# Performance work log

Hardware: AMD Instinct MI355X
Metric: run time of the kernel (lower is better)

The kernel has to match this reference:

```python
import jax, jax.numpy as jnp
import numpy as np

N_NODES = 100000
N_EDGES = 1600000
IN_CH = 512
MID_CH = 64   # hard-coded mid_layer_channel in the module
OUT_CH = 40


def setup_inputs() -> dict:
    key = jax.random.key(0)
    k0, k1, k2, k3 = jax.random.split(key, 4)
    node_feature = jax.random.normal(k0, (N_NODES, IN_CH), dtype=jnp.float32)
    # edge index [2, E]: row 0 = src, row 1 = dst
    adj_list = jax.random.randint(k1, (2, N_EDGES), 0, N_NODES, dtype=jnp.int32)
    # GCNConv parameters (Glorot-ish scale)
    W1 = jax.random.normal(k2, (IN_CH, MID_CH), dtype=jnp.float32) * (1.0 / np.sqrt(IN_CH))
    b1 = jnp.zeros((MID_CH,), dtype=jnp.float32)
    W2 = jax.random.normal(k3, (MID_CH, OUT_CH), dtype=jnp.float32) * (1.0 / np.sqrt(MID_CH))
    b2 = jnp.zeros((OUT_CH,), dtype=jnp.float32)
    return {"node_feature": node_feature, "adj_list": adj_list,
            "W1": W1, "b1": b1, "W2": W2, "b2": b2}


def _gcn_conv(x, W, b, src, dst, deg_inv_sqrt, n_nodes):
    # Standard GCNConv: D^{-1/2} (A + I) D^{-1/2} (x W) + b
    h = x @ W                                             # [N, F_out]
    norm = deg_inv_sqrt[src] * deg_inv_sqrt[dst]          # [E]
    agg = jax.ops.segment_sum(h[src] * norm[:, None], dst, num_segments=n_nodes)
    agg = agg + h * (deg_inv_sqrt * deg_inv_sqrt)[:, None]  # self-loop term
    return agg + b


def reference(node_feature, adj_list, W1, b1, W2, b2):
    n = node_feature.shape[0]
    src, dst = adj_list[0], adj_list[1]
    # degree with self-loops (in-degree at dst + 1)
    deg = jax.ops.segment_sum(jnp.ones_like(dst, dtype=node_feature.dtype), dst,
                              num_segments=n) + 1.0
    deg_inv_sqrt = jax.lax.rsqrt(deg)
    h = jax.nn.elu(_gcn_conv(node_feature, W1, b1, src, dst, deg_inv_sqrt, n))
    out = _gcn_conv(h, W2, b2, src, dst, deg_inv_sqrt, n)
    return jax.nn.log_softmax(out, axis=1)
```

## Files before the change

kernel.cpp:

```cpp
#include <hip/hip_runtime.h>
#include <hip/hip_bf16.h>
#include <math.h>

#define IN_CH 512
#define MID_CH 64
#define OUT_CH 40

typedef __attribute__((ext_vector_type(8))) short short8;
typedef __attribute__((ext_vector_type(4))) float f32x4;
typedef __attribute__((ext_vector_type(2))) float f32x2;

static __device__ __forceinline__ unsigned short f2bf(float f) {
    unsigned int u = __float_as_uint(f);
    u += 0x7fffu + ((u >> 16) & 1u);
    return (unsigned short)(u >> 16);
}

__global__ void k_init(const float* __restrict__ W1, unsigned short* __restrict__ w1f,
                       int* __restrict__ cnt, int* __restrict__ esrc, int dummy_off,
                       int epad, unsigned char* __restrict__ h1q,
                       unsigned char* __restrict__ h2q, int N) {
    int i = blockIdx.x * 256 + threadIdx.x;
    if (i < epad) esrc[i] = dummy_off;
    if (i < N) cnt[i] = 0;
    if (i < IN_CH * MID_CH) {
        int k = i >> 6, c = i & 63;
        w1f[(((k >> 3) * 64) + c) * 8 + (k & 7)] = f2bf(W1[i]);
    }
    if (i < 64) {
        h1q[(size_t)N * 64 + i] = 0;
        h2q[(size_t)N * 64 + i] = 0;
    }
}

__global__ void k_count(const int* __restrict__ dst, int* __restrict__ cnt, int E) {
    int i = blockIdx.x * blockDim.x + threadIdx.x;
    if (i < E) atomicAdd(&cnt[dst[i]], 1);
}

__global__ void k_scanA(const int* __restrict__ cnt, int* __restrict__ rowptr,
                        int* __restrict__ bsum, float* __restrict__ dis, int N) {
    __shared__ int wsum[16];
    int i = blockIdx.x * 1024 + threadIdx.x;
    int lane = threadIdx.x & 63, wv = threadIdx.x >> 6;
    int v = (i < N) ? cnt[i] : 0;
    if (i < N) dis[i] = rsqrtf((float)v + 1.0f);
    int x = (v + 3) & ~3;
    #pragma unroll
    for (int off = 1; off < 64; off <<= 1) {
        int t = __shfl_up(x, off);
        if (lane >= off) x += t;
    }
    if (lane == 63) wsum[wv] = x;
    __syncthreads();
    if (wv == 0 && lane < 16) {
        int own = wsum[lane];
        int y = own;
        #pragma unroll
        for (int off = 1; off < 16; off <<= 1) {
            int t = __shfl_up(y, off);
            if (lane >= off) y += t;
        }
        wsum[lane] = y - own;
        if (lane == 15) bsum[blockIdx.x] = y;
    }
    __syncthreads();
    if (i < N) rowptr[i + 1] = x + wsum[wv];
}

__global__ void k_scanB(int* __restrict__ bsum, int nb) {
    __shared__ int tmp[2];
    int lane = threadIdx.x & 63, wv = threadIdx.x >> 6;
    int v = (threadIdx.x < nb) ? bsum[threadIdx.x] : 0;
    int x = v;
    #pragma unroll
    for (int off = 1; off < 64; off <<= 1) {
        int t = __shfl_up(x, off);
        if (lane >= off) x += t;
    }
    if (lane == 63) tmp[wv] = x;
    __syncthreads();
    int add = (wv == 1) ? tmp[0] : 0;
    if (threadIdx.x < nb) bsum[threadIdx.x] = x - v + add;
}

__global__ void k_scanC(int* __restrict__ rowptr, int* __restrict__ cur,
                        const int* __restrict__ bsum, int N) {
    int i = blockIdx.x * 1024 + threadIdx.x;
    if (i < N) {
        int v = rowptr[i + 1] + bsum[blockIdx.x];
        rowptr[i + 1] = v;
        cur[i + 1] = v;
    }
    if (i == 0) { rowptr[0] = 0; cur[0] = 0; }
}

__launch_bounds__(256, 6)
__global__ void k_fillgemm(const float* __restrict__ X, const unsigned short* __restrict__ w1f,
                           const float* __restrict__ dis, unsigned char* __restrict__ h1q,
                           int N, int FB,
                           const int* __restrict__ src, const int* __restrict__ dst,
                           int* __restrict__ cur, int* __restrict__ esrc, int E) {
    if ((int)blockIdx.x < FB) {
        int fb = blockIdx.x;
        int pb = fb & 7;
        int ch = fb >> 3;
        int nch = FB >> 3;
        int ech = (E + nch - 1) / nch;
        int e0 = ch * ech;
        int e1 = e0 + ech; if (e1 > E) e1 = E;
        #pragma unroll 4
        for (int e = e0 + (int)threadIdx.x; e < e1; e += 256) {
            int d = dst[e];
            if ((d & 7) == pb) {
                int p = atomicAdd(&cur[d], 1);
                esrc[p] = src[e] << 6;
            }
        }
        return;
    }

    int wave = threadIdx.x >> 6, lane = threadIdx.x & 63;
    int gb = blockIdx.x - FB;
    int rbase = gb * 64 + wave * 16;
    int g = lane >> 4;
    int arow = rbase + (lane & 15);
    if (arow > N - 1) arow = N - 1;
    const float* xp = X + (size_t)arow * IN_CH + g * 8;
    const short8* wb = (const short8*)w1f;

    f32x4 acc[4];
    #pragma unroll
    for (int i = 0; i < 4; ++i) acc[i] = (f32x4){0.f, 0.f, 0.f, 0.f};

    float4 bx0[2], bx1[2];
    {
        const float4* p0 = (const float4*)(xp);
        const float4* p1 = (const float4*)(xp + 32);
        bx0[0] = p0[0]; bx1[0] = p0[1];
        bx0[1] = p1[0]; bx1[1] = p1[1];
    }

    #pragma unroll
    for (int ks = 0; ks < 16; ++ks) {
        float4 x0 = bx0[ks & 1], x1 = bx1[ks & 1];
        if (ks < 14) {
            const float4* p = (const float4*)(xp + (ks + 2) * 32);
            bx0[ks & 1] = p[0]; bx1[ks & 1] = p[1];
        }
        short8 a;
        a[0] = (short)f2bf(x0.x); a[1] = (short)f2bf(x0.y);
        a[2] = (short)f2bf(x0.z); a[3] = (short)f2bf(x0.w);
        a[4] = (short)f2bf(x1.x); a[5] = (short)f2bf(x1.y);
        a[6] = (short)f2bf(x1.z); a[7] = (short)f2bf(x1.w);

        int cibase = (ks * 4 + g) * 64 + (lane & 15);
        #pragma unroll
        for (int ct = 0; ct < 4; ++ct) {
            short8 b = wb[cibase + ct * 16];
            acc[ct] = __builtin_amdgcn_mfma_f32_16x16x32_bf16(a, b, acc[ct], 0, 0, 0);
        }
    }

    int colb = lane & 15;
    int rquad = rbase + (lane >> 4) * 4;
    #pragma unroll
    for (int ct = 0; ct < 4; ++ct) {
        #pragma unroll
        for (int r = 0; r < 4; ++r) {
            int row = rquad + r;
            if (row < N) {
                float v = acc[ct][r] * dis[row];
                unsigned q = __builtin_amdgcn_cvt_pk_fp8_f32(v, v, 0, false);
                h1q[(size_t)row * 64 + ct * 16 + colb] = (unsigned char)q;
            }
        }
    }
}

#define AGG_UNPACK8(Q)                                              \
    {                                                               \
        f32x2 lo_ = __builtin_amdgcn_cvt_pk_f32_fp8((Q), false);    \
        f32x2 hi_ = __builtin_amdgcn_cvt_pk_f32_fp8((Q), true);     \
        acc[0] += lo_[0]; acc[1] += lo_[1];                         \
        acc[2] += hi_[0]; acc[3] += hi_[1];                         \
    }

#define GATHER_CORE(HB)                                                 \
    f32x4 acc = (f32x4){0.f, 0.f, 0.f, 0.f};                            \
    for (int cbeg = beg; cbeg < end; cbeg += 64) {                      \
        int m = end - cbeg; if (m > 64) m = 64;      \
        int soff = esrc[cbeg + lane];                                   \
        int k4n = m >> 2;                                               \
        int k4 = 0;                                                     \
        for (; k4 + 4 <= k4n; k4 += 4) {                                \
            int o0 = __shfl(soff, (k4 + 0) * 4 + g);                    \
            int o1 = __shfl(soff, (k4 + 1) * 4 + g);                    \
            int o2 = __shfl(soff, (k4 + 2) * 4 + g);                    \
            int o3 = __shfl(soff, (k4 + 3) * 4 + g);                    \
            unsigned q0 = *(const unsigned*)((HB) + ((unsigned)o0 + cgoff)); \
            unsigned q1 = *(const unsigned*)((HB) + ((unsigned)o1 + cgoff)); \
            unsigned q2 = *(const unsigned*)((HB) + ((unsigned)o2 + cgoff)); \
            unsigned q3 = *(const unsigned*)((HB) + ((unsigned)o3 + cgoff)); \
            AGG_UNPACK8(q0) AGG_UNPACK8(q1) AGG_UNPACK8(q2) AGG_UNPACK8(q3) \
        }                                                               \
        for (; k4 < k4n; ++k4) {                                        \
            int o = __shfl(soff, k4 * 4 + g);                           \
            unsigned q = *(const unsigned*)((HB) + ((unsigned)o + cgoff)); \
            AGG_UNPACK8(q)                                              \
        }                                                               \
    }                                                                   \
    _Pragma("unroll")                                                   \
    for (int off = 32; off >= 16; off >>= 1) {                          \
        acc[0] += __shfl_xor(acc[0], off);                              \
        acc[1] += __shfl_xor(acc[1], off);                              \
        acc[2] += __shfl_xor(acc[2], off);                              \
        acc[3] += __shfl_xor(acc[3], off);                              \
    }

__launch_bounds__(256)
__global__ void k_agg1(const unsigned char* __restrict__ hq, const float* __restrict__ dis,
                       const int* __restrict__ rowptr, const int* __restrict__ esrc,
                       const float* __restrict__ b1, unsigned char* __restrict__ h2q,
                       int N) {
    int wv = threadIdx.x >> 6, lane = threadIdx.x & 63;
    int n = blockIdx.x * 4 + wv;
    if (n >= N) return;
    int g = lane >> 4, cg = lane & 15;
    int beg = rowptr[n], end = rowptr[n + 1];
    unsigned cgoff = (unsigned)(cg * 4);
    const char* hb = (const char*)hq;

    GATHER_CORE(hb)

    if (g == 0) {
        float dn = dis[n];
        unsigned qs = *(const unsigned*)(hb + ((unsigned)(n * 64) + cgoff));
        f32x2 slo = __builtin_amdgcn_cvt_pk_f32_fp8(qs, false);
        f32x2 shi = __builtin_amdgcn_cvt_pk_f32_fp8(qs, true);
        float4 b4 = *(const float4*)(b1 + cg * 4);
        float v0 = dn * (acc[0] + slo[0]) + b4.x;
        float v1 = dn * (acc[1] + slo[1]) + b4.y;
        float v2 = dn * (acc[2] + shi[0]) + b4.z;
        float v3 = dn * (acc[3] + shi[1]) + b4.w;
        v0 = v0 > 0.f ? v0 : expm1f(v0);
        v1 = v1 > 0.f ? v1 : expm1f(v1);
        v2 = v2 > 0.f ? v2 : expm1f(v2);
        v3 = v3 > 0.f ? v3 : expm1f(v3);
        unsigned w = __builtin_amdgcn_cvt_pk_fp8_f32(dn * v0, dn * v1, 0, false);
        w = __builtin_amdgcn_cvt_pk_fp8_f32(dn * v2, dn * v3, w, true);
        *(unsigned*)(h2q + (size_t)n * 64 + cg * 4) = w;
    }
}

__launch_bounds__(256)
__global__ void k_agg2(const unsigned char* __restrict__ hq, const float* __restrict__ dis,
                       const int* __restrict__ rowptr, const int* __restrict__ esrc,
                       const float* __restrict__ W2, const float* __restrict__ b2,
                       float* __restrict__ out, int N) {
    __shared__ float w2l[MID_CH * OUT_CH];
    __shared__ float vl[4 * MID_CH];
    for (int f = threadIdx.x; f < MID_CH * OUT_CH; f += 256) w2l[f] = W2[f];
    __syncthreads();

    int wv = threadIdx.x >> 6, lane = threadIdx.x & 63;
    int n = blockIdx.x * 4 + wv;
    if (n >= N) return;
    int g = lane >> 4, cg = lane & 15;
    int beg = rowptr[n], end = rowptr[n + 1];
    unsigned cgoff = (unsigned)(cg * 4);
    const char* hb = (const char*)hq;

    GATHER_CORE(hb)

    if (g == 0) {
        float dn = dis[n];
        unsigned qs = *(const unsigned*)(hb + ((unsigned)(n * 64) + cgoff));
        f32x2 slo = __builtin_amdgcn_cvt_pk_f32_fp8(qs, false);
        f32x2 shi = __builtin_amdgcn_cvt_pk_f32_fp8(qs, true);
        float4 v;
        v.x = dn * (acc[0] + slo[0]);
        v.y = dn * (acc[1] + slo[1]);
        v.z = dn * (acc[2] + shi[0]);
        v.w = dn * (acc[3] + shi[1]);
        *(float4*)&vl[wv * 64 + cg * 4] = v;
    }

    float o = (lane < OUT_CH) ? b2[lane] : 0.f;
    const float* vrow = &vl[wv * 64];
    #pragma unroll 8
    for (int c = 0; c < MID_CH; ++c)
        o += vrow[c] * w2l[c * OUT_CH + lane];

    float mx = (lane < OUT_CH) ? o : -1e30f;
    #pragma unroll
    for (int off = 32; off > 0; off >>= 1) mx = fmaxf(mx, __shfl_xor(mx, off));
    float e = (lane < OUT_CH) ? expf(o - mx) : 0.f;
    float ssum = e;
    #pragma unroll
    for (int off = 32; off > 0; off >>= 1) ssum += __shfl_xor(ssum, off);
    if (lane < OUT_CH)
        out[(size_t)n * OUT_CH + lane] = o - mx - logf(ssum);
}

extern "C" void kernel_launch(void* const* d_in, const int* in_sizes, int n_in,
                              void* d_out, int out_size, void* d_ws, size_t ws_size,
                              hipStream_t stream) {
    const float* X  = (const float*)d_in[0];
    const int* adj  = (const int*)d_in[1];
    const float* W1 = (const float*)d_in[2];
    const float* b1 = (const float*)d_in[3];
    const float* W2 = (const float*)d_in[4];
    const float* b2 = (const float*)d_in[5];
    float* out = (float*)d_out;

    int N = in_sizes[0] / IN_CH;
    int E = in_sizes[1] / 2;
    const int* srcp = adj;
    const int* dstp = adj + E;
    int nchunk = (N + 1023) / 1024;
    int epad_max = E + 3 * N + 128;
    int FB = 1024;
    int GB = (N + 63) / 64;

    char* ws = (char*)d_ws;
    size_t off = 0;
    int*   cnt    = (int*)(ws + off);  off += (size_t)N * sizeof(int);
    int*   cur    = (int*)(ws + off);  off += ((size_t)N + 8) * sizeof(int);
    float* dis    = (float*)(ws + off); off += (size_t)N * sizeof(float);
    int*   rowptr = (int*)(ws + off);  off += ((size_t)N + 8) * sizeof(int);
    int*   bsum   = (int*)(ws + off);  off += 128 * sizeof(int);
    int*   esrc   = (int*)(ws + off);  off += (size_t)epad_max * sizeof(int);
    unsigned short* w1f = (unsigned short*)(ws + off); off += (size_t)IN_CH * MID_CH * sizeof(unsigned short);
    unsigned char* h1q = (unsigned char*)(ws + off); off += (size_t)(N + 4) * MID_CH;
    unsigned char* h2q = (unsigned char*)(ws + off); off += (size_t)(N + 4) * MID_CH;

    k_init<<<(epad_max + 255) / 256, 256, 0, stream>>>(W1, w1f, cnt, esrc, N << 6,
                                                       epad_max, h1q, h2q, N);
    k_count<<<(E + 255) / 256, 256, 0, stream>>>(dstp, cnt, E);
    k_scanA<<<nchunk, 1024, 0, stream>>>(cnt, rowptr, bsum, dis, N);
    k_scanB<<<1, 128, 0, stream>>>(bsum, nchunk);
    k_scanC<<<nchunk, 1024, 0, stream>>>(rowptr, cur, bsum, N);

    k_fillgemm<<<FB + GB, 256, 0, stream>>>(X, w1f, dis, h1q, N, FB,
                                            srcp, dstp, cur, esrc, E);

    int nb = (N + 3) / 4;
    k_agg1<<<nb, 256, 0, stream>>>(h1q, dis, rowptr, esrc, b1, h2q, N);
    k_agg2<<<nb, 256, 0, stream>>>(h2q, dis, rowptr, esrc, W2, b2, out, N);
}
```

Before: 326.7 us.

## Split fused fill/GEMM kernel and stage W1 in LDS with deeper prefetch

Splits the combined CSR-fill and first-layer GEMM kernel into two separate kernels. The fill becomes a simple grid-stride atomic scatter, dropping the dst-modulo-8 partitioning. The GEMM now uses 512-thread blocks that copy the full bf16 W1 (64KB) into shared memory, read B fragments from LDS, and prefetch four X chunks instead of two. This cuts repeated global/L2 reads of W1, but the fill no longer overlaps the GEMM and the 64KB LDS per block limits occupancy.

```diff
diff --git a/kernel.cpp b/kernel.cpp
--- a/kernel.cpp
+++ b/kernel.cpp
@@ -95,58 +95,54 @@
     if (i == 0) { rowptr[0] = 0; cur[0] = 0; }
 }
 
-__launch_bounds__(256, 6)
-__global__ void k_fillgemm(const float* __restrict__ X, const unsigned short* __restrict__ w1f,
-                           const float* __restrict__ dis, unsigned char* __restrict__ h1q,
-                           int N, int FB,
-                           const int* __restrict__ src, const int* __restrict__ dst,
-                           int* __restrict__ cur, int* __restrict__ esrc, int E) {
-    if ((int)blockIdx.x < FB) {
-        int fb = blockIdx.x;
-        int pb = fb & 7;
-        int ch = fb >> 3;
-        int nch = FB >> 3;
-        int ech = (E + nch - 1) / nch;
-        int e0 = ch * ech;
-        int e1 = e0 + ech; if (e1 > E) e1 = E;
-        #pragma unroll 4
-        for (int e = e0 + (int)threadIdx.x; e < e1; e += 256) {
-            int d = dst[e];
-            if ((d & 7) == pb) {
-                int p = atomicAdd(&cur[d], 1);
-                esrc[p] = src[e] << 6;
-            }
-        }
-        return;
-    }
+__global__ void k_fill(const int* __restrict__ src, const int* __restrict__ dst,
+                       int* __restrict__ cur, int* __restrict__ esrc, int E) {
+    int i = blockIdx.x * blockDim.x + threadIdx.x;
+    int stride = gridDim.x * blockDim.x;
+    for (int e = i; e < E; e += stride) {
+        int p = atomicAdd(&cur[dst[e]], 1);
+        esrc[p] = src[e] << 6;
+    }
+}
+
+__launch_bounds__(512, 4)
+__global__ void k_gemm1(const float* __restrict__ X, const unsigned short* __restrict__ w1f,
+                        const float* __restrict__ dis, unsigned char* __restrict__ h1q,
+                        int N) {
+    __shared__ __align__(16) unsigned short wlds[IN_CH * MID_CH];
+    {
+        const uint4* s4 = (const uint4*)w1f;
+        uint4* d4 = (uint4*)wlds;
+        #pragma unroll
+        for (int i = 0; i < 8; ++i)
+            d4[threadIdx.x + i * 512] = s4[threadIdx.x + i * 512];
+    }
+    __syncthreads();
 
     int wave = threadIdx.x >> 6, lane = threadIdx.x & 63;
-    int gb = blockIdx.x - FB;
-    int rbase = gb * 64 + wave * 16;
+    int rbase = blockIdx.x * 128 + wave * 16;
     int g = lane >> 4;
     int arow = rbase + (lane & 15);
     if (arow > N - 1) arow = N - 1;
     const float* xp = X + (size_t)arow * IN_CH + g * 8;
-    const short8* wb = (const short8*)w1f;
 
     f32x4 acc[4];
     #pragma unroll
     for (int i = 0; i < 4; ++i) acc[i] = (f32x4){0.f, 0.f, 0.f, 0.f};
 
-    float4 bx0[2], bx1[2];
-    {
-        const float4* p0 = (const float4*)(xp);
-        const float4* p1 = (const float4*)(xp + 32);
-        bx0[0] = p0[0]; bx1[0] = p0[1];
-        bx0[1] = p1[0]; bx1[1] = p1[1];
+    float4 bx0[4], bx1[4];
+    #pragma unroll
+    for (int i = 0; i < 4; ++i) {
+        const float4* p = (const float4*)(xp + i * 32);
+        bx0[i] = p[0]; bx1[i] = p[1];
     }
 
     #pragma unroll
     for (int ks = 0; ks < 16; ++ks) {
-        float4 x0 = bx0[ks & 1], x1 = bx1[ks & 1];
-        if (ks < 14) {
-            const float4* p = (const float4*)(xp + (ks + 2) * 32);
-            bx0[ks & 1] = p[0]; bx1[ks & 1] = p[1];
+        float4 x0 = bx0[ks & 3], x1 = bx1[ks & 3];
+        if (ks < 12) {
+            const float4* p = (const float4*)(xp + (ks + 4) * 32);
+            bx0[ks & 3] = p[0]; bx1[ks & 3] = p[1];
         }
         short8 a;
         a[0] = (short)f2bf(x0.x); a[1] = (short)f2bf(x0.y);
@@ -157,7 +153,7 @@
         int cibase = (ks * 4 + g) * 64 + (lane & 15);
         #pragma unroll
         for (int ct = 0; ct < 4; ++ct) {
-            short8 b = wb[cibase + ct * 16];
+            short8 b = *((const short8*)(wlds + (size_t)(cibase + ct * 16) * 8));
             acc[ct] = __builtin_amdgcn_mfma_f32_16x16x32_bf16(a, b, acc[ct], 0, 0, 0);
         }
     }
@@ -320,8 +316,6 @@
     const int* dstp = adj + E;
     int nchunk = (N + 1023) / 1024;
     int epad_max = E + 3 * N + 128;
-    int FB = 1024;
-    int GB = (N + 63) / 64;
 
     char* ws = (char*)d_ws;
     size_t off = 0;
@@ -342,8 +336,8 @@
     k_scanB<<<1, 128, 0, stream>>>(bsum, nchunk);
     k_scanC<<<nchunk, 1024, 0, stream>>>(rowptr, cur, bsum, N);
 
-    k_fillgemm<<<FB + GB, 256, 0, stream>>>(X, w1f, dis, h1q, N, FB,
-                                            srcp, dstp, cur, esrc, E);
+    k_fill<<<2048, 256, 0, stream>>>(srcp, dstp, cur, esrc, E);
+    k_gemm1<<<(N + 127) / 128, 512, 0, stream>>>(X, w1f, dis, h1q, N);
 
     int nb = (N + 3) / 4;
     k_agg1<<<nb, 256, 0, stream>>>(h1q, dis, rowptr, esrc, b1, h2q, N);
```

New measurement: 366.3 us. +12.1%, slower.
